# Kernel tuning notes

Measured on AMD Instinct MI355X. Metric: run time of the kernel, lower is better.

Reference implementation:

```python
import jax, jax.numpy as jnp
import numpy as np
from functools import partial

B, S, H = 4, 2048, 1152
NH, HD = 12, 96          # heads, head_dim
NM, MD = 4, 128          # memory heads (indices 6..9), mem_dim
K = 4                    # base kernel
STRIDE = 64              # NeuralMemory chunk stride
INNER = 4 * H            # GLU inner dim
CS_DIL = (1, 2, 4, 8, 16, 32)  # DilatedConvStack: config.dilations[:6]
HEAD_DIL = ((1, 2, 4), (1, 1, 1), (4, 8, 16), (8, 16, 32), (32, 64, 128),
            (64, 128, 256), (256, 512, 1024), (1, 100, 200), (1, 500, 1000),
            (1, 1024, 2048), (3, 9, 27), (5, 25, 125))
MEM_HEADS = (6, 7, 8, 9)


def setup_inputs() -> dict:
    key = jax.random.key(0)
    ks = iter(jax.random.split(key, 48))
    def nrm(shape, s=0.02):
        return jax.random.normal(next(ks), shape, jnp.float32) * s
    return {
        'x': jax.random.normal(next(ks), (B, S, H), jnp.float32),
        'norm1_w': jnp.ones((H,), jnp.float32),
        'norm2_w': jnp.ones((H,), jnp.float32),
        'norm3_w': jnp.ones((H,), jnp.float32),
        'cs_w': nrm((6, H, K), 0.1), 'cs_b': jnp.zeros((6, H), jnp.float32),
        'cs_proj_w': nrm((H, H)), 'cs_proj_b': jnp.zeros((H,), jnp.float32),
        'gate_proj_w': nrm((H, 2 * H)),
        'router_w': nrm((H, NH)), 'router_b': jnp.zeros((NH,), jnp.float32),
        'head_w': nrm((NH, 3, HD, K), 0.1), 'head_b': jnp.zeros((NH, 3, HD), jnp.float32),
        'mem_q': nrm((NM, HD, HD), 0.01), 'mem_k': nrm((NM, HD, HD), 0.01),
        'mem_v': nrm((NM, HD, MD), 0.01), 'mem_gw': nrm((NM, HD)),
        'mem_gb': jnp.full((NM,), -2.0, jnp.float32), 'mem_out': nrm((NM, MD, HD), 0.01),
        'mixgate_w': nrm((H, H)), 'mixgate_b': jnp.full((H,), 2.0, jnp.float32),
        'mixing_w': nrm((H, H)), 'mixing_b': jnp.zeros((H,), jnp.float32),
        'ffn_in_w': nrm((H, 2 * INNER)), 'ffn_out_w': nrm((INNER, H)),
        'cg_w': nrm((H,)), 'cg_b': jnp.float32(1.0),
        'sg_w': nrm((H,)), 'sg_b': jnp.float32(1.0),
        'fg_w': nrm((H,)), 'fg_b': jnp.float32(1.0),
    }


def rmsnorm(x, w, eps=1e-6):
    n = jax.lax.rsqrt(jnp.mean(x * x, axis=-1, keepdims=True) + eps)
    return x * n * w


def dconv(x, w, b, d):
    """Depthwise causal dilated conv. x:[B,S,C], w:[C,K], b:[C]."""
    s = x.shape[1]
    pad = (w.shape[1] - 1) * d
    xp = jnp.pad(x, ((0, 0), (pad, 0), (0, 0)))
    acc = b
    for j in range(w.shape[1]):
        acc = acc + w[:, j] * jax.lax.dynamic_slice_in_dim(xp, j * d, s, axis=1)
    return acc


def conv_stack(x, cs_w, cs_b, proj_w, proj_b):
    h = x
    for i, d in enumerate(CS_DIL):
        h = h + jax.nn.gelu(dconv(h, cs_w[i], cs_b[i], d), approximate=False)
    return h @ proj_w + proj_b


def neural_memory(xm, Wq, Wk, Wv, gw, gb, Wout):
    """Chunked fast-weight memory for NM heads at once. xm:[B,S,NM,HD]."""
    q = jnp.einsum('bsnd,nde->bsne', xm, Wq)
    k = jnp.einsum('bsnd,nde->bsne', xm, Wk)
    v = jnp.einsum('bsnd,ndm->bsnm', xm, Wv)
    g = jax.nn.sigmoid(jnp.einsum('bsnd,nd->bsn', xm, gw) + gb)[..., None]  # [B,S,NM,1]
    nC = S // STRIDE
    def chunk(a):  # [B,S,...] -> [nC,B,STRIDE,...]
        return a.reshape(B, nC, STRIDE, *a.shape[2:]).swapaxes(0, 1)
    q_c, kg_c, v_c = chunk(q), chunk(k * g), chunk(v)
    ga_c = chunk(g).mean(axis=2)[..., None]  # [nC,B,NM,1,1]
    M0 = jnp.zeros((B, NM, HD, MD), xm.dtype)
    def step(M, xs):
        qc, kc, vc, ga = xs
        reads = jnp.einsum('bsnd,bndm->bsnm', qc, M)
        write = jnp.einsum('bsnd,bsnm->bndm', kc, vc)
        return (1.0 - ga) * M + write, reads
    _, reads = jax.lax.scan(step, M0, (q_c, kg_c, v_c, ga_c))
    reads = reads.swapaxes(0, 1).reshape(B, S, NM, MD)
    return jnp.einsum('bsnm,nmd->bsnd', reads, Wout)


def multi_head_state(x, gate_proj_w, router_w, router_b, head_w, head_b,
                     mem_q, mem_k, mem_v, mem_gw, mem_gb, mem_out,
                     mixgate_w, mixgate_b, mixing_w, mixing_b):
    head_weights = jax.nn.sigmoid(x @ router_w + router_b)  # [B,S,NH]
    gp = x @ gate_proj_w
    xg = gp[..., :H] * jax.nn.sigmoid(gp[..., H:])
    xh = xg.reshape(B, S, NH, HD)
    outs = []
    for i in range(NH):
        h = xh[:, :, i, :]
        for j, d in enumerate(HEAD_DIL[i]):
            h = h + dconv(h, head_w[i, j], head_b[i, j], d)
        outs.append(h)
    mem = neural_memory(xh[:, :, MEM_HEADS[0]:MEM_HEADS[-1] + 1, :],
                        mem_q, mem_k, mem_v, mem_gw, mem_gb, mem_out)
    for n, i in enumerate(MEM_HEADS):
        outs[i] = outs[i] + mem[:, :, n, :]
    out = jnp.stack(outs, axis=2) * head_weights[..., None]
    out = out.reshape(B, S, H)
    out = out * jax.nn.sigmoid(out @ mixgate_w + mixgate_b)
    return out @ mixing_w + mixing_b


def glu(x, win, wout):
    h = x @ win
    return (h[..., :INNER] * jax.nn.sigmoid(h[..., INNER:])) @ wout


def reference(x, norm1_w, norm2_w, norm3_w, cs_w, cs_b, cs_proj_w, cs_proj_b,
              gate_proj_w, router_w, router_b, head_w, head_b,
              mem_q, mem_k, mem_v, mem_gw, mem_gb, mem_out,
              mixgate_w, mixgate_b, mixing_w, mixing_b,
              ffn_in_w, ffn_out_w, cg_w, cg_b, sg_w, sg_b, fg_w, fg_b):
    gc = jax.nn.sigmoid(x @ cg_w + cg_b)[..., None]
    x = x + gc * conv_stack(rmsnorm(x, norm1_w), cs_w, cs_b, cs_proj_w, cs_proj_b)
    gs = jax.nn.sigmoid(x @ sg_w + sg_b)[..., None]
    x = x + gs * multi_head_state(rmsnorm(x, norm2_w), gate_proj_w, router_w, router_b,
                                  head_w, head_b, mem_q, mem_k, mem_v, mem_gw, mem_gb,
                                  mem_out, mixgate_w, mixgate_b, mixing_w, mixing_b)
    gf = jax.nn.sigmoid(x @ fg_w + fg_b)[..., None]
    x = x + gf * glu(rmsnorm(x, norm3_w), ffn_in_w, ffn_out_w)
    return x
```

## Files before the change

### kernel.cpp

```cpp
#include <hip/hip_runtime.h>
#include <hip/hip_bf16.h>
#include <math.h>

#define TOKENS 8192
#define HDIM 1152
#define SEQ 2048
#define NHEADS 12
#define HEADD 96
#define NMEM 4
#define MEMD 128
#define FINNER 4608

typedef __hip_bfloat16 bf16;
typedef __attribute__((ext_vector_type(8))) short short8;
typedef __attribute__((ext_vector_type(4))) float floatx4;

__device__ __constant__ int g_hd_dil[NHEADS * 3] = {
    1, 2, 4,   1, 1, 1,    4, 8, 16,   8, 16, 32,
    32, 64, 128, 64, 128, 256, 256, 512, 1024, 1, 100, 200,
    1, 500, 1000, 1, 1024, 2048, 3, 9, 27, 5, 25, 125};

__device__ inline float sigm(float x) { return 1.0f / (1.0f + __expf(-x)); }
__device__ inline float gelu_exact(float x) {
  return 0.5f * x * (1.0f + erff(x * 0.70710678118654752f));
}
__device__ inline float wred(float v) {
#pragma unroll
  for (int o = 32; o > 0; o >>= 1) v += __shfl_down(v, o);
  return v;
}
__device__ inline void gl_lds16(const bf16* g, bf16* l) {
  __builtin_amdgcn_global_load_lds(
      (const __attribute__((address_space(1))) unsigned int*)g,
      (__attribute__((address_space(3))) unsigned int*)l, 16, 0, 0);
}

__global__ __launch_bounds__(256) void k_transpose_bf16(
    const float* __restrict__ W, bf16* __restrict__ WT, int K, int N) {
  __shared__ float t[32][33];
  int k0 = blockIdx.y * 32, n0 = blockIdx.x * 32;
  int tx = threadIdx.x & 31, ty = threadIdx.x >> 5;
#pragma unroll
  for (int i = 0; i < 32; i += 8)
    t[ty + i][tx] = W[(size_t)(k0 + ty + i) * N + (n0 + tx)];
  __syncthreads();
#pragma unroll
  for (int i = 0; i < 32; i += 8)
    WT[(size_t)(n0 + ty + i) * K + (k0 + tx)] = __float2bfloat16(t[tx][ty + i]);
}

__global__ __launch_bounds__(256) void k_transpose_pair(
    const float* __restrict__ W, bf16* __restrict__ WT, int K, int N) {
  __shared__ float t[32][33];
  int half = N >> 1;
  int k0 = blockIdx.y * 32, n0 = blockIdx.x * 32;
  int tx = threadIdx.x & 31, ty = threadIdx.x >> 5;
  int c = (tx < 16) ? (n0 / 2 + tx) : (half + n0 / 2 + tx - 16);
#pragma unroll
  for (int i = 0; i < 32; i += 8)
    t[ty + i][tx] = W[(size_t)(k0 + ty + i) * N + c];
  __syncthreads();
#pragma unroll
  for (int i = 0; i < 32; i += 8) {
    int r = ty + i;
    WT[(size_t)(n0 + r) * K + (k0 + tx)] = __float2bfloat16(t[tx][r]);
  }
}

__global__ __launch_bounds__(256) void k_rms_gate(
    const float* __restrict__ x, const float* __restrict__ nw,
    const float* __restrict__ gw, const float* __restrict__ gb,
    bf16* __restrict__ outb, float* __restrict__ gout,
    const float* __restrict__ rw, const float* __restrict__ rb,
    float* __restrict__ hwout) {
  int wave = threadIdx.x >> 6, lane = threadIdx.x & 63;
  int tok = blockIdx.x * 4 + wave;
  const float* row = x + (size_t)tok * HDIM;
  float2 a[9];
  float s2 = 0.f, gd = 0.f;
#pragma unroll
  for (int p = 0; p < 9; ++p) {
    int i2 = lane + 64 * p;
    a[p] = *reinterpret_cast<const float2*>(&row[i2 * 2]);
    float2 g2 = *reinterpret_cast<const float2*>(&gw[i2 * 2]);
    s2 += a[p].x * a[p].x + a[p].y * a[p].y;
    gd += a[p].x * g2.x + a[p].y * g2.y;
  }
  s2 = wred(s2);
  gd = wred(gd);
  if (lane == 0) gout[tok] = sigm(gd + gb[0]);
  s2 = __shfl(s2, 0);
  float rn = 1.0f / sqrtf(s2 / (float)HDIM + 1e-6f);
  float racc[NHEADS];
#pragma unroll
  for (int o = 0; o < NHEADS; ++o) racc[o] = 0.f;
#pragma unroll
  for (int p = 0; p < 9; ++p) {
    int i2 = lane + 64 * p;
    float2 w2 = *reinterpret_cast<const float2*>(&nw[i2 * 2]);
    float nx = a[p].x * rn * w2.x;
    float ny = a[p].y * rn * w2.y;
    __hip_bfloat162 pr;
    pr.x = __float2bfloat16(nx);
    pr.y = __float2bfloat16(ny);
    *reinterpret_cast<__hip_bfloat162*>(&outb[(size_t)tok * HDIM + i2 * 2]) = pr;
    if (hwout) {
      const float4* rp4 =
          reinterpret_cast<const float4*>(&rw[(size_t)(i2 * 2) * NHEADS]);
      float4 r0 = rp4[0], r1 = rp4[1], r2 = rp4[2];
      float4 r3 = rp4[3], r4 = rp4[4], r5 = rp4[5];
      racc[0] += nx * r0.x + ny * r3.x;
      racc[1] += nx * r0.y + ny * r3.y;
      racc[2] += nx * r0.z + ny * r3.z;
      racc[3] += nx * r0.w + ny * r3.w;
      racc[4] += nx * r1.x + ny * r4.x;
      racc[5] += nx * r1.y + ny * r4.y;
      racc[6] += nx * r1.z + ny * r4.z;
      racc[7] += nx * r1.w + ny * r4.w;
      racc[8] += nx * r2.x + ny * r5.x;
      racc[9] += nx * r2.y + ny * r5.y;
      racc[10] += nx * r2.z + ny * r5.z;
      racc[11] += nx * r2.w + ny * r5.w;
    }
  }
  if (hwout) {
#pragma unroll
    for (int o = 0; o < NHEADS; ++o) {
      float r = wred(racc[o]);
      if (lane == 0) hwout[(size_t)tok * NHEADS + o] = sigm(r + rb[o]);
    }
  }
}

#define CS_T 256
#define CS_HALO 189
#define CS_ROWS 445
#define CS_J2 14
__global__ __launch_bounds__(256) void k_convstack(
    const bf16* __restrict__ hin, bf16* __restrict__ outb,
    const float* __restrict__ cw, const float* __restrict__ cb) {
  __shared__ float cur[CS_ROWS * 16];
  int bx = blockIdx.x;
  int cs = bx % 72;
  int tile = (bx / 72) & 7;
  int b = bx / 576;
  int c0 = cs * 16;
  int S0 = tile * CS_T;
  int tid = threadIdx.x;
  int c4 = tid & 7, pg = tid >> 3;
  for (int i = tid; i < CS_ROWS * 8; i += 256) {
    int p = i >> 3, cc2 = (i & 7) * 2;
    int sg = S0 - CS_HALO + p;
    if (sg >= 0) {
      unsigned int u = *reinterpret_cast<const unsigned int*>(
          &hin[((size_t)(b * SEQ + sg)) * HDIM + c0 + cc2]);
      cur[p * 16 + cc2] = __uint_as_float(u << 16);
      cur[p * 16 + cc2 + 1] = __uint_as_float(u & 0xffff0000u);
    } else {
      cur[p * 16 + cc2] = 0.f;
      cur[p * 16 + cc2 + 1] = 0.f;
    }
  }
  const int dil[6] = {1, 2, 4, 8, 16, 32};
  const int Nk[6] = {3, 9, 21, 45, 93, 189};
  float2 nv[CS_J2];
#pragma unroll
  for (int k = 0; k < 6; ++k) {
    int dd = dil[k] * 16;
    const float4* wp = reinterpret_cast<const float4*>(
        &cw[((size_t)k * HDIM + c0 + c4 * 2) * 4]);
    float4 wA = wp[0], wB = wp[1];
    float2 bb = *reinterpret_cast<const float2*>(&cb[(size_t)k * HDIM + c0 + c4 * 2]);
    __syncthreads();
#pragma unroll
    for (int j = 0; j < CS_J2; ++j) {
      int p = pg + 32 * j;
      if (p >= Nk[k] && p < CS_ROWS) {
        int i = p * 16 + c4 * 2;
        float2 t3 = *reinterpret_cast<const float2*>(&cur[i - 3 * dd]);
        float2 t2 = *reinterpret_cast<const float2*>(&cur[i - 2 * dd]);
        float2 t1 = *reinterpret_cast<const float2*>(&cur[i - dd]);
        float2 t0 = *reinterpret_cast<const float2*>(&cur[i]);
        float acc0 = bb.x + wA.x * t3.x + wA.y * t2.x + wA.z * t1.x + wA.w * t0.x;
        float acc1 = bb.y + wB.x * t3.y + wB.y * t2.y + wB.z * t1.y + wB.w * t0.y;
        int sg = S0 - CS_HALO + p;
        if (sg >= 0) {
          nv[j].x = t0.x + gelu_exact(acc0);
          nv[j].y = t0.y + gelu_exact(acc1);
        } else {
          nv[j].x = 0.f;
          nv[j].y = 0.f;
        }
      }
    }
    __syncthreads();
#pragma unroll
    for (int j = 0; j < CS_J2; ++j) {
      int p = pg + 32 * j;
      if (p >= Nk[k] && p < CS_ROWS)
        *reinterpret_cast<float2*>(&cur[p * 16 + c4 * 2]) = nv[j];
    }
  }
  __syncthreads();
  for (int r = pg; r < CS_T; r += 32) {
    float2 v2 = *reinterpret_cast<const float2*>(&cur[(CS_HALO + r) * 16 + c4 * 2]);
    __hip_bfloat162 pr;
    pr.x = __float2bfloat16(v2.x);
    pr.y = __float2bfloat16(v2.y);
    *reinterpret_cast<__hip_bfloat162*>(
        &outb[((size_t)(b * SEQ + S0 + r)) * HDIM + c0 + c4 * 2]) = pr;
  }
}

__global__ __launch_bounds__(256) void k_headconv(
    const float* __restrict__ hin, float* __restrict__ hout,
    const float* __restrict__ hw_, const float* __restrict__ hb_, int j) {
  size_t idx4 = (size_t)blockIdx.x * 256 + threadIdx.x;
  if (idx4 >= (size_t)TOKENS * HDIM / 4) return;
  size_t idx = idx4 * 4;
  int c = (int)(idx % HDIM);
  int head = c / HEADD, hd = c % HEADD;
  size_t tok = idx / HDIM;
  int s = (int)(tok % SEQ);
  int d = g_hd_dil[head * 3 + j];
  const float4* wv = reinterpret_cast<const float4*>(
      hw_ + ((size_t)(head * 3 + j) * HEADD + hd) * 4);
  float4 w0 = wv[0], w1 = wv[1], w2 = wv[2], w3 = wv[3];
  float4 bb = *reinterpret_cast<const float4*>(
      &hb_[(size_t)(head * 3 + j) * HEADD + hd]);
  float av0 = bb.x, av1 = bb.y, av2 = bb.z, av3 = bb.w;
  float4 base = *reinterpret_cast<const float4*>(&hin[idx]);
#pragma unroll
  for (int jj = 0; jj < 4; ++jj) {
    int back = (3 - jj) * d;
    if (s - back >= 0) {
      float4 t = *reinterpret_cast<const float4*>(&hin[idx - (size_t)back * HDIM]);
      float a0 = (jj == 0) ? w0.x : (jj == 1) ? w0.y : (jj == 2) ? w0.z : w0.w;
      float a1 = (jj == 0) ? w1.x : (jj == 1) ? w1.y : (jj == 2) ? w1.z : w1.w;
      float a2 = (jj == 0) ? w2.x : (jj == 1) ? w2.y : (jj == 2) ? w2.z : w2.w;
      float a3 = (jj == 0) ? w3.x : (jj == 1) ? w3.y : (jj == 2) ? w3.z : w3.w;
      av0 += a0 * t.x;
      av1 += a1 * t.y;
      av2 += a2 * t.z;
      av3 += a3 * t.w;
    }
  }
  float4 o = {base.x + av0, base.y + av1, base.z + av2, base.w + av3};
  *reinterpret_cast<float4*>(&hout[idx]) = o;
}

template <int MODE>
__global__ __launch_bounds__(256) void k_gemm(
    const bf16* __restrict__ A, const bf16* __restrict__ BT,
    const float* __restrict__ bias, const float* __restrict__ gate,
    const float* addin, float* outf, bf16* outb, int M, int N, int K) {
  __shared__ bf16 As[128 * 64];
  __shared__ bf16 Bs[128 * 64];
  const int tid = threadIdx.x;
  const int m0 = blockIdx.y * 128, n0 = blockIdx.x * 128;
  const int wave = tid >> 6, lane = tid & 63;
  const int wm = (wave & 1) * 64, wn = (wave >> 1) * 64;
  const int l16 = lane & 15, kq = lane >> 4;
  const int srow = lane >> 3;
  const int schunk = ((lane & 7) - srow) & 7;
  const bf16* gA = A + (size_t)(m0 + wave * 32 + srow) * K + schunk * 8;
  const bf16* gB = BT + (size_t)(n0 + wave * 32 + srow) * K + schunk * 8;
  bf16* lA = &As[wave * 32 * 64];
  bf16* lB = &Bs[wave * 32 * 64];
  const size_t rstride = (size_t)8 * K;
  const int col0 = ((kq + l16) & 7) * 8;
  const int col1 = ((kq + 4 + l16) & 7) * 8;
  floatx4 acc[4][4];
  floatx4 zero = {0.f, 0.f, 0.f, 0.f};
#pragma unroll
  for (int i = 0; i < 4; ++i)
#pragma unroll
    for (int jj = 0; jj < 4; ++jj) acc[i][jj] = zero;

  for (int k0 = 0; k0 < K; k0 += 64) {
    __syncthreads();
#pragma unroll
    for (int i = 0; i < 4; ++i) {
      gl_lds16(gA + k0 + i * rstride, lA + i * 8 * 64);
      gl_lds16(gB + k0 + i * rstride, lB + i * 8 * 64);
    }
    __syncthreads();
#pragma unroll
    for (int ks = 0; ks < 2; ++ks) {
      const int col = ks ? col1 : col0;
      short8 af[4], bfr[4];
#pragma unroll
      for (int t = 0; t < 4; ++t) {
        af[t] = *reinterpret_cast<const short8*>(&As[(wm + t * 16 + l16) * 64 + col]);
        bfr[t] = *reinterpret_cast<const short8*>(&Bs[(wn + t * 16 + l16) * 64 + col]);
      }
#pragma unroll
      for (int mt = 0; mt < 4; ++mt)
#pragma unroll
        for (int nt = 0; nt < 4; ++nt)
          acc[mt][nt] = __builtin_amdgcn_mfma_f32_16x16x32_bf16(
              af[mt], bfr[nt], acc[mt][nt], 0, 0, 0);
    }
  }

  if (MODE == 4 || MODE == 5) {
    const int halfN = N >> 1;
#pragma unroll
    for (int mt = 0; mt < 4; ++mt) {
#pragma unroll
      for (int ntp = 0; ntp < 2; ++ntp) {
        int cc = ((n0 + wn) >> 1) + ntp * 16 + l16;
#pragma unroll
        for (int r = 0; r < 4; ++r) {
          float a = acc[mt][ntp * 2][r];
          float g = acc[mt][ntp * 2 + 1][r];
          int m = m0 + wm + mt * 16 + kq * 4 + r;
          float res = a * sigm(g);
          size_t o = (size_t)m * halfN + cc;
          if (MODE == 4) outf[o] = res;
          else outb[o] = __float2bfloat16(res);
        }
      }
    }
    return;
  }

#pragma unroll
  for (int mt = 0; mt < 4; ++mt) {
#pragma unroll
    for (int nt = 0; nt < 4; ++nt) {
      int n = n0 + wn + nt * 16 + l16;
      float bv = bias ? bias[n] : 0.f;
#pragma unroll
      for (int r = 0; r < 4; ++r) {
        int m = m0 + wm + mt * 16 + kq * 4 + r;
        float v = acc[mt][nt][r] + bv;
        size_t o = (size_t)m * N + n;
        if (MODE == 2) outf[o] = addin[o] + gate[m] * v;
        else if (MODE == 6) outb[o] = __float2bfloat16(addin[o] * sigm(v));
      }
    }
  }
}

#define QT 16
#define QTP 20
__global__ __launch_bounds__(256) void k_qkvg(
    const float* __restrict__ xh, const float* __restrict__ Wq,
    const float* __restrict__ Wk, const float* __restrict__ Wv,
    const float* __restrict__ gw, const float* __restrict__ gb,
    float* __restrict__ q, float* __restrict__ kg, float* __restrict__ v,
    float* __restrict__ gout) {
  __shared__ float xT[384 * QTP];
  __shared__ float gsh[QT][NMEM];
  int bx = blockIdx.x;
  int grp = bx & 1;
  int tile = bx >> 1;
  int t0 = tile * QT;
  int tid = threadIdx.x;
  for (int i = tid; i < 384 * QT; i += 256) {
    int t = i / 384, dd = i % 384;
    xT[dd * QTP + t] = xh[(size_t)(t0 + t) * HDIM + 6 * HEADD + dd];
  }
  __syncthreads();
  if (grp == 0) {
    if (tid < 64) {
      int t = tid >> 2, n = tid & 3;
      float a = gb[n];
      for (int d = 0; d < HEADD; ++d)
        a += xT[(n * HEADD + d) * QTP + t] * gw[n * HEADD + d];
      float s = sigm(a);
      gsh[t][n] = s;
      gout[(size_t)(t0 + t) * NMEM + n] = s;
    }
    __syncthreads();
  }
  int o = grp * 1024 + tid * 4;
  if (o >= 1280) return;
  float acc[4][QT];
#pragma unroll
  for (int e = 0; e < 4; ++e)
#pragma unroll
    for (int t = 0; t < QT; ++t) acc[e][t] = 0.f;

  if (o < 768) {
    int qk = (o >= 384) ? 1 : 0;
    int oo = o - qk * 384;
    int n = oo / HEADD, eb = oo % HEADD;
    const float* W = (qk ? Wk : Wq) + (size_t)n * HEADD * HEADD;
    const int ddb = n * HEADD;
    for (int d = 0; d < HEADD; ++d) {
      float4 w4 = *reinterpret_cast<const float4*>(&W[(size_t)d * HEADD + eb]);
      const float* xr = &xT[(ddb + d) * QTP];
#pragma unroll
      for (int tq = 0; tq < QT / 4; ++tq) {
        float4 xv = *reinterpret_cast<const float4*>(&xr[tq * 4]);
        float xa[4] = {xv.x, xv.y, xv.z, xv.w};
#pragma unroll
        for (int u = 0; u < 4; ++u) {
          acc[0][tq * 4 + u] += xa[u] * w4.x;
          acc[1][tq * 4 + u] += xa[u] * w4.y;
          acc[2][tq * 4 + u] += xa[u] * w4.z;
          acc[3][tq * 4 + u] += xa[u] * w4.w;
        }
      }
    }
    if (qk == 0) {
#pragma unroll
      for (int t = 0; t < QT; ++t) {
        float4 ov = {acc[0][t], acc[1][t], acc[2][t], acc[3][t]};
        *reinterpret_cast<float4*>(&q[(size_t)(t0 + t) * 384 + oo]) = ov;
      }
    } else {
#pragma unroll
      for (int t = 0; t < QT; ++t) {
        float g = gsh[t][n];
        float4 ov = {acc[0][t] * g, acc[1][t] * g, acc[2][t] * g, acc[3][t] * g};
        *reinterpret_cast<float4*>(&kg[(size_t)(t0 + t) * 384 + oo]) = ov;
      }
    }
  } else {
    int i2 = o - 768;
    int n = i2 / MEMD, eb = i2 % MEMD;
    const float* W = Wv + (size_t)n * HEADD * MEMD;
    const int ddb = n * HEADD;
    for (int d = 0; d < HEADD; ++d) {
      float4 w4 = *reinterpret_cast<const float4*>(&W[(size_t)d * MEMD + eb]);
      const float* xr = &xT[(ddb + d) * QTP];
#pragma unroll
      for (int tq = 0; tq < QT / 4; ++tq) {
        float4 xv = *reinterpret_cast<const float4*>(&xr[tq * 4]);
        float xa[4] = {xv.x, xv.y, xv.z, xv.w};
#pragma unroll
        for (int u = 0; u < 4; ++u) {
          acc[0][tq * 4 + u] += xa[u] * w4.x;
          acc[1][tq * 4 + u] += xa[u] * w4.y;
          acc[2][tq * 4 + u] += xa[u] * w4.z;
          acc[3][tq * 4 + u] += xa[u] * w4.w;
        }
      }
    }
#pragma unroll
    for (int t = 0; t < QT; ++t) {
      float4 ov = {acc[0][t], acc[1][t], acc[2][t], acc[3][t]};
      *reinterpret_cast<float4*>(&v[(size_t)(t0 + t) * 512 + i2]) = ov;
    }
  }
}

__global__ __launch_bounds__(256) void k_memW(const float* __restrict__ kg,
                                              const float* __restrict__ v,
                                              float* __restrict__ W) {
  __shared__ float X[64 * 96];
  __shared__ float V[64 * 128];
  int bx = blockIdx.x;
  int bn = bx >> 5, ch = bx & 31;
  int b = bn >> 2, n = bn & 3;
  int t0 = b * SEQ + ch * 64;
  int tid = threadIdx.x;
  for (int i = tid; i < 64 * 96; i += 256) {
    int s = i / 96, d = i % 96;
    X[i] = kg[((size_t)(t0 + s) * NMEM + n) * HEADD + d];
  }
  for (int i = tid; i < 64 * 128; i += 256) {
    int s = i >> 7, m = i & 127;
    V[i] = v[((size_t)(t0 + s) * NMEM + n) * MEMD + m];
  }
  __syncthreads();
  float* Wb = W + (size_t)bx * 96 * 128;
  for (int t = tid; t < 768; t += 256) {
    int d0 = (t >> 5) * 4, m0 = (t & 31) * 4;
    float acc[4][4] = {};
    for (int s = 0; s < 64; ++s) {
      float4 xv = *reinterpret_cast<const float4*>(&X[s * 96 + d0]);
      float4 vv = *reinterpret_cast<const float4*>(&V[s * 128 + m0]);
      float xa[4] = {xv.x, xv.y, xv.z, xv.w};
      float va[4] = {vv.x, vv.y, vv.z, vv.w};
#pragma unroll
      for (int a = 0; a < 4; ++a)
#pragma unroll
        for (int e = 0; e < 4; ++e) acc[a][e] += xa[a] * va[e];
    }
#pragma unroll
    for (int a = 0; a < 4; ++a) {
      float4 o = {acc[a][0], acc[a][1], acc[a][2], acc[a][3]};
      *reinterpret_cast<float4*>(&Wb[(size_t)(d0 + a) * 128 + m0]) = o;
    }
  }
}

__global__ __launch_bounds__(256) void k_memscanM(const float* __restrict__ W,
                                                  const float* __restrict__ g,
                                                  float* __restrict__ Mp) {
  __shared__ float ga_sh[32];
  int bx = blockIdx.x;
  int bn = bx / 48, j = bx % 48;
  int elem = j * 256 + threadIdx.x;
  int b = bn >> 2, n = bn & 3;
  int tid = threadIdx.x;
  {
    int ch = tid >> 3, i8 = tid & 7;
    float s = 0.f;
#pragma unroll
    for (int t = 0; t < 8; ++t)
      s += g[((size_t)b * SEQ + ch * 64 + i8 * 8 + t) * NMEM + n];
#pragma unroll
    for (int o = 4; o > 0; o >>= 1) s += __shfl_down(s, o);
    if (i8 == 0) ga_sh[ch] = s * (1.0f / 64.0f);
  }
  __syncthreads();
  float wreg[32];
  size_t base0 = (size_t)bn * 32 * 12288 + elem;
#pragma unroll
  for (int ch = 0; ch < 32; ++ch) wreg[ch] = W[base0 + (size_t)ch * 12288];
  float M = 0.f;
#pragma unroll
  for (int ch = 0; ch < 32; ++ch) {
    Mp[base0 + (size_t)ch * 12288] = M;
    M = (1.f - ga_sh[ch]) * M + wreg[ch];
  }
}

__global__ __launch_bounds__(256) void k_memR(const float* __restrict__ q,
                                              const float* __restrict__ Mp,
                                              const float* __restrict__ Wout,
                                              float* __restrict__ rdp) {
  extern __shared__ float smem[];
  float* Q = smem;
  float* Ms = smem + 64 * 96;
  int bx = blockIdx.x;
  int bn = bx >> 5, ch = bx & 31;
  int b = bn >> 2, n = bn & 3;
  int t0 = b * SEQ + ch * 64;
  int tid = threadIdx.x;
  for (int i = tid; i < 64 * 96; i += 256) {
    int s = i / 96, d = i % 96;
    Q[i] = q[((size_t)(t0 + s) * NMEM + n) * HEADD + d];
  }
  for (int i = tid; i < 96 * 128; i += 256)
    Ms[i] = Mp[((size_t)bn * 32 + ch) * 12288 + i];
  __syncthreads();
  float acc[2][4][4];
#pragma unroll
  for (int tt = 0; tt < 2; ++tt) {
    int t = tid + tt * 256;
    int s0 = (t >> 5) * 4, m0 = (t & 31) * 4;
#pragma unroll
    for (int si = 0; si < 4; ++si)
#pragma unroll
      for (int mi = 0; mi < 4; ++mi) acc[tt][si][mi] = 0.f;
    for (int k = 0; k < 96; ++k) {
      float4 mv = *reinterpret_cast<const float4*>(&Ms[k * 128 + m0]);
      float ma[4] = {mv.x, mv.y, mv.z, mv.w};
#pragma unroll
      for (int si = 0; si < 4; ++si) {
        float qs = Q[(s0 + si) * 96 + k];
#pragma unroll
        for (int mi = 0; mi < 4; ++mi) acc[tt][si][mi] += qs * ma[mi];
      }
    }
  }
  __syncthreads();
  float* reads_s = smem;
#pragma unroll
  for (int tt = 0; tt < 2; ++tt) {
    int t = tid + tt * 256;
    int s0 = (t >> 5) * 4, m0 = (t & 31) * 4;
#pragma unroll
    for (int si = 0; si < 4; ++si) {
      float4 o = {acc[tt][si][0], acc[tt][si][1], acc[tt][si][2], acc[tt][si][3]};
      *reinterpret_cast<float4*>(&reads_s[(s0 + si) * 128 + m0]) = o;
    }
  }
  __syncthreads();
  const float* Wn = Wout + (size_t)n * MEMD * HEADD;
  for (int it = tid; it < 64 * 24; it += 256) {
    int s = it / 24, c4 = (it % 24) * 4;
    float p0 = 0.f, p1 = 0.f, p2 = 0.f, p3 = 0.f;
    for (int m = 0; m < MEMD; ++m) {
      float rv = reads_s[s * 128 + m];
      float4 w4 = *reinterpret_cast<const float4*>(&Wn[(size_t)m * HEADD + c4]);
      p0 += rv * w4.x;
      p1 += rv * w4.y;
      p2 += rv * w4.z;
      p3 += rv * w4.w;
    }
    float4 o = {p0, p1, p2, p3};
    *reinterpret_cast<float4*>(
        &rdp[((size_t)(t0 + s) * NMEM + n) * HEADD + c4]) = o;
  }
}

__global__ __launch_bounds__(256) void k_combine(
    const float* __restrict__ hconv, const float* __restrict__ rdp,
    const float* __restrict__ hw, float* __restrict__ outf,
    bf16* __restrict__ outb) {
  size_t idx4 = (size_t)blockIdx.x * 256 + threadIdx.x;
  if (idx4 >= (size_t)TOKENS * HDIM / 4) return;
  size_t idx = idx4 * 4;
  int c = (int)(idx % HDIM);
  size_t tok = idx / HDIM;
  int head = c / HEADD, hd = c % HEADD;
  float4 v = *reinterpret_cast<const float4*>(&hconv[idx]);
  if (head >= 6 && head < 10) {
    float4 r = *reinterpret_cast<const float4*>(
        &rdp[((size_t)tok * NMEM + (head - 6)) * HEADD + hd]);
    v.x += r.x;
    v.y += r.y;
    v.z += r.z;
    v.w += r.w;
  }
  float w = hw[tok * NHEADS + head];
  v.x *= w;
  v.y *= w;
  v.z *= w;
  v.w *= w;
  *reinterpret_cast<float4*>(&outf[idx]) = v;
  __hip_bfloat162 p01, p23;
  p01.x = __float2bfloat16(v.x);
  p01.y = __float2bfloat16(v.y);
  p23.x = __float2bfloat16(v.z);
  p23.y = __float2bfloat16(v.w);
  *reinterpret_cast<__hip_bfloat162*>(&outb[idx]) = p01;
  *reinterpret_cast<__hip_bfloat162*>(&outb[idx + 2]) = p23;
}

extern "C" void kernel_launch(void* const* d_in, const int* in_sizes, int n_in,
                              void* d_out, int out_size, void* d_ws,
                              size_t ws_size, hipStream_t stream) {
  const float* x_in = (const float*)d_in[0];
  const float* norm1_w = (const float*)d_in[1];
  const float* norm2_w = (const float*)d_in[2];
  const float* norm3_w = (const float*)d_in[3];
  const float* cs_w = (const float*)d_in[4];
  const float* cs_b = (const float*)d_in[5];
  const float* cs_proj_w = (const float*)d_in[6];
  const float* cs_proj_b = (const float*)d_in[7];
  const float* gate_proj_w = (const float*)d_in[8];
  const float* router_w = (const float*)d_in[9];
  const float* router_b = (const float*)d_in[10];
  const float* head_w = (const float*)d_in[11];
  const float* head_b = (const float*)d_in[12];
  const float* mem_q = (const float*)d_in[13];
  const float* mem_k = (const float*)d_in[14];
  const float* mem_v = (const float*)d_in[15];
  const float* mem_gw = (const float*)d_in[16];
  const float* mem_gb = (const float*)d_in[17];
  const float* mem_out = (const float*)d_in[18];
  const float* mixgate_w = (const float*)d_in[19];
  const float* mixgate_b = (const float*)d_in[20];
  const float* mixing_w = (const float*)d_in[21];
  const float* mixing_b = (const float*)d_in[22];
  const float* ffn_in_w = (const float*)d_in[23];
  const float* ffn_out_w = (const float*)d_in[24];
  const float* cg_w = (const float*)d_in[25];
  const float* cg_b = (const float*)d_in[26];
  const float* sg_w = (const float*)d_in[27];
  const float* sg_b = (const float*)d_in[28];
  const float* fg_w = (const float*)d_in[29];
  const float* fg_b = (const float*)d_in[30];
  float* out = (float*)d_out;

  char* wsp = (char*)d_ws;
  size_t off = 0;
  auto alloc = [&](size_t bytes) -> char* {
    char* p = wsp + off;
    off += (bytes + 255) & ~(size_t)255;
    return p;
  };
  bf16* NB = (bf16*)alloc((size_t)TOKENS * HDIM * 2);
  float* F1 = (float*)alloc((size_t)TOKENS * HDIM * 4);
  float* F2 = (float*)alloc((size_t)TOKENS * HDIM * 4);
  float* F3 = (float*)alloc((size_t)TOKENS * HDIM * 4);
  char* REG = alloc((size_t)TOKENS * FINNER * 2);
  float* qb = (float*)REG;
  float* kgb = (float*)(REG + (size_t)TOKENS * 384 * 4);
  float* vb = (float*)((char*)kgb + (size_t)TOKENS * 384 * 4);
  float* rdb = (float*)((char*)vb + (size_t)TOKENS * 512 * 4);
  bf16* XG = (bf16*)REG;
  bf16* NB2 = (bf16*)REG;
  bf16* NBc = (bf16*)REG;
  bf16* WTcs = (bf16*)alloc((size_t)1152 * 1152 * 2);
  bf16* WTgp = (bf16*)alloc((size_t)2304 * 1152 * 2);
  bf16* WTmg = (bf16*)alloc((size_t)1152 * 1152 * 2);
  bf16* WTmx = (bf16*)alloc((size_t)1152 * 1152 * 2);
  float* G1 = (float*)alloc(TOKENS * 4);
  float* G2 = (float*)alloc(TOKENS * 4);
  float* G3 = (float*)alloc(TOKENS * 4);
  float* GM = (float*)alloc((size_t)TOKENS * NMEM * 4);
  float* HW = (float*)alloc((size_t)TOKENS * NHEADS * 4);
  bf16* WTfin = (bf16*)F1;
  bf16* WTfout = (bf16*)F2;
  float* Wbuf = F2;
  float* Mpref = F3;

  const int gE4 = (TOKENS * HDIM) / (4 * 256);

  k_transpose_bf16<<<dim3(36, 36), 256, 0, stream>>>(cs_proj_w, WTcs, 1152, 1152);
  k_transpose_pair<<<dim3(72, 36), 256, 0, stream>>>(gate_proj_w, WTgp, 1152, 2304);
  k_transpose_bf16<<<dim3(36, 36), 256, 0, stream>>>(mixgate_w, WTmg, 1152, 1152);
  k_transpose_bf16<<<dim3(36, 36), 256, 0, stream>>>(mixing_w, WTmx, 1152, 1152);

  k_rms_gate<<<2048, 256, 0, stream>>>(x_in, norm1_w, cg_w, cg_b, NB, G1,
                                       nullptr, nullptr, nullptr);
  k_convstack<<<2304, 256, 0, stream>>>(NB, NBc, cs_w, cs_b);
  k_gemm<2><<<dim3(9, 64), 256, 0, stream>>>(NBc, WTcs, cs_proj_b, G1, x_in, out,
                                             nullptr, TOKENS, 1152, 1152);

  k_rms_gate<<<2048, 256, 0, stream>>>(out, norm2_w, sg_w, sg_b, NB, G2,
                                       router_w, router_b, HW);
  k_gemm<4><<<dim3(18, 64), 256, 0, stream>>>(NB, WTgp, nullptr, nullptr, nullptr,
                                              F3, nullptr, TOKENS, 2304, 1152);
  k_headconv<<<gE4, 256, 0, stream>>>(F3, F1, head_w, head_b, 0);
  k_headconv<<<gE4, 256, 0, stream>>>(F1, F2, head_w, head_b, 1);
  k_headconv<<<gE4, 256, 0, stream>>>(F2, F1, head_w, head_b, 2);
  k_qkvg<<<1024, 256, 0, stream>>>(F3, mem_q, mem_k, mem_v, mem_gw, mem_gb,
                                   qb, kgb, vb, GM);
  k_memW<<<512, 256, 0, stream>>>(kgb, vb, Wbuf);
  k_memscanM<<<768, 256, 0, stream>>>(Wbuf, GM, Mpref);
  k_memR<<<512, 256, (64 * 96 + 96 * 128) * 4, stream>>>(qb, Mpref, mem_out, rdb);
  k_combine<<<gE4, 256, 0, stream>>>(F1, rdb, HW, F2, NB);
  k_gemm<6><<<dim3(9, 64), 256, 0, stream>>>(NB, WTmg, mixgate_b, nullptr, F2,
                                             nullptr, NB2, TOKENS, 1152, 1152);
  k_gemm<2><<<dim3(9, 64), 256, 0, stream>>>(NB2, WTmx, mixing_b, G2, out, out,
                                             nullptr, TOKENS, 1152, 1152);

  k_rms_gate<<<2048, 256, 0, stream>>>(out, norm3_w, fg_w, fg_b, NB, G3,
                                       nullptr, nullptr, nullptr);
  k_transpose_pair<<<dim3(288, 36), 256, 0, stream>>>(ffn_in_w, WTfin, 1152, 9216);
  k_transpose_bf16<<<dim3(36, 144), 256, 0, stream>>>(ffn_out_w, WTfout, 4608, 1152);
  k_gemm<5><<<dim3(72, 64), 256, 0, stream>>>(NB, WTfin, nullptr, nullptr, nullptr,
                                              nullptr, XG, TOKENS, 9216, 1152);
  k_gemm<2><<<dim3(9, 64), 256, 0, stream>>>(XG, WTfout, nullptr, G3, out, out,
                                             nullptr, TOKENS, 1152, 4608);
}
```

Baseline: 1.264 ms.

## Fuse three per-head dilated convolutions into one LDS-resident kernel

Replaces three separate elementwise head-conv launches, each reading and writing the full fp32 activation through global memory, with a single kernel. That kernel loads a full sequence for four channels of one batch into shared memory, applies all three dilated causal conv stages in place, and writes the result once. This removes two full round trips of the intermediate tensor and two launches. In exchange, each block handles a 48KB LDS tile with strided 8-byte global accesses (four channels per row), which lowers occupancy and coalescing.

```diff
diff --git a/kernel.cpp b/kernel.cpp
--- a/kernel.cpp
+++ b/kernel.cpp
@@ -212,41 +212,73 @@
   }
 }
 
-__global__ __launch_bounds__(256) void k_headconv(
+#define HC_S 6
+__global__ __launch_bounds__(256) void k_headconv3(
     const float* __restrict__ hin, float* __restrict__ hout,
-    const float* __restrict__ hw_, const float* __restrict__ hb_, int j) {
-  size_t idx4 = (size_t)blockIdx.x * 256 + threadIdx.x;
-  if (idx4 >= (size_t)TOKENS * HDIM / 4) return;
-  size_t idx = idx4 * 4;
-  int c = (int)(idx % HDIM);
-  int head = c / HEADD, hd = c % HEADD;
-  size_t tok = idx / HDIM;
-  int s = (int)(tok % SEQ);
-  int d = g_hd_dil[head * 3 + j];
-  const float4* wv = reinterpret_cast<const float4*>(
-      hw_ + ((size_t)(head * 3 + j) * HEADD + hd) * 4);
-  float4 w0 = wv[0], w1 = wv[1], w2 = wv[2], w3 = wv[3];
-  float4 bb = *reinterpret_cast<const float4*>(
-      &hb_[(size_t)(head * 3 + j) * HEADD + hd]);
-  float av0 = bb.x, av1 = bb.y, av2 = bb.z, av3 = bb.w;
-  float4 base = *reinterpret_cast<const float4*>(&hin[idx]);
-#pragma unroll
-  for (int jj = 0; jj < 4; ++jj) {
-    int back = (3 - jj) * d;
-    if (s - back >= 0) {
-      float4 t = *reinterpret_cast<const float4*>(&hin[idx - (size_t)back * HDIM]);
-      float a0 = (jj == 0) ? w0.x : (jj == 1) ? w0.y : (jj == 2) ? w0.z : w0.w;
-      float a1 = (jj == 0) ? w1.x : (jj == 1) ? w1.y : (jj == 2) ? w1.z : w1.w;
-      float a2 = (jj == 0) ? w2.x : (jj == 1) ? w2.y : (jj == 2) ? w2.z : w2.w;
-      float a3 = (jj == 0) ? w3.x : (jj == 1) ? w3.y : (jj == 2) ? w3.z : w3.w;
-      av0 += a0 * t.x;
-      av1 += a1 * t.y;
-      av2 += a2 * t.z;
-      av3 += a3 * t.w;
-    }
-  }
-  float4 o = {base.x + av0, base.y + av1, base.z + av2, base.w + av3};
-  *reinterpret_cast<float4*>(&hout[idx]) = o;
+    const float* __restrict__ hw_, const float* __restrict__ hb_) {
+  __shared__ float cur[SEQ * HC_S];
+  int bx = blockIdx.x;
+  int b = bx / 288;
+  int grp = bx % 288;
+  int c0 = grp * 4;
+  int head = c0 / HEADD;
+  int hd0 = c0 % HEADD;
+  int tid = threadIdx.x;
+  int pr = tid & 1, rg = tid >> 1;
+  for (int i = tid; i < SEQ * 2; i += 256) {
+    int s = i >> 1, pp = i & 1;
+    float2 v = *reinterpret_cast<const float2*>(
+        &hin[((size_t)(b * SEQ + s)) * HDIM + c0 + pp * 2]);
+    *reinterpret_cast<float2*>(&cur[s * HC_S + pp * 2]) = v;
+  }
+  float2 nv[16];
+#pragma unroll
+  for (int j = 0; j < 3; ++j) {
+    int d = g_hd_dil[head * 3 + j];
+    const float4* wp = reinterpret_cast<const float4*>(
+        &hw_[((size_t)(head * 3 + j) * HEADD + hd0 + pr * 2) * 4]);
+    float4 wA = wp[0], wB = wp[1];
+    float2 bb = *reinterpret_cast<const float2*>(
+        &hb_[(size_t)(head * 3 + j) * HEADD + hd0 + pr * 2]);
+    __syncthreads();
+#pragma unroll
+    for (int jj = 0; jj < 16; ++jj) {
+      int p = rg + 128 * jj;
+      float2 t0 = *reinterpret_cast<const float2*>(&cur[p * HC_S + pr * 2]);
+      float a0 = bb.x + wA.w * t0.x;
+      float a1 = bb.y + wB.w * t0.y;
+      if (p - d >= 0) {
+        float2 t = *reinterpret_cast<const float2*>(&cur[(p - d) * HC_S + pr * 2]);
+        a0 += wA.z * t.x;
+        a1 += wB.z * t.y;
+      }
+      if (p - 2 * d >= 0) {
+        float2 t = *reinterpret_cast<const float2*>(&cur[(p - 2 * d) * HC_S + pr * 2]);
+        a0 += wA.y * t.x;
+        a1 += wB.y * t.y;
+      }
+      if (p - 3 * d >= 0) {
+        float2 t = *reinterpret_cast<const float2*>(&cur[(p - 3 * d) * HC_S + pr * 2]);
+        a0 += wA.x * t.x;
+        a1 += wB.x * t.y;
+      }
+      nv[jj].x = t0.x + a0;
+      nv[jj].y = t0.y + a1;
+    }
+    __syncthreads();
+#pragma unroll
+    for (int jj = 0; jj < 16; ++jj) {
+      int p = rg + 128 * jj;
+      *reinterpret_cast<float2*>(&cur[p * HC_S + pr * 2]) = nv[jj];
+    }
+  }
+  __syncthreads();
+  for (int i = tid; i < SEQ * 2; i += 256) {
+    int s = i >> 1, pp = i & 1;
+    float2 v = *reinterpret_cast<const float2*>(&cur[s * HC_S + pp * 2]);
+    *reinterpret_cast<float2*>(
+        &hout[((size_t)(b * SEQ + s)) * HDIM + c0 + pp * 2]) = v;
+  }
 }
 
 template <int MODE>
@@ -711,9 +743,7 @@
                                        router_w, router_b, HW);
   k_gemm<4><<<dim3(18, 64), 256, 0, stream>>>(NB, WTgp, nullptr, nullptr, nullptr,
                                               F3, nullptr, TOKENS, 2304, 1152);
-  k_headconv<<<gE4, 256, 0, stream>>>(F3, F1, head_w, head_b, 0);
-  k_headconv<<<gE4, 256, 0, stream>>>(F1, F2, head_w, head_b, 1);
-  k_headconv<<<gE4, 256, 0, stream>>>(F2, F1, head_w, head_b, 2);
+  k_headconv3<<<1152, 256, 0, stream>>>(F3, F1, head_w, head_b);
   k_qkvg<<<1024, 256, 0, stream>>>(F3, mem_q, mem_k, mem_v, mem_gw, mem_gb,
                                    qb, kgb, vb, GM);
   k_memW<<<512, 256, 0, stream>>>(kgb, vb, Wbuf);
```

Result: faster. 1.152 ms (-8.9%).
